# Kernel optimization log

Hardware: AMD Instinct MI355X
Metric: run time of the kernel (lower is better)

The kernel has to match this reference:

```python
import jax, jax.numpy as jnp
import numpy as np

N = 100000   # nodes
E = 800000   # edges
NC = 500     # category nodes
EC = 20000   # category relation edges
D = 64       # out_feats
HOUR_PERIOD = 6  # emb_mix('hour') uses time_period = 6


def l2norm(x):
    # torch F.normalize(p=2, dim=-1) with eps clamp
    return x / jnp.maximum(jnp.linalg.norm(x, axis=-1, keepdims=True), 1e-12)


def proj_transh(x, norm):
    # x - <x, norm> * norm  (per-row)
    return x - jnp.sum(x * norm, axis=-1, keepdims=True) * norm


def edge_softmax(score, dst, n):
    # softmax over incoming edges of each destination node
    m = jax.ops.segment_max(score, dst, num_segments=n)
    e = jnp.exp(score - m[dst])
    s = jax.ops.segment_sum(e, dst, num_segments=n)
    return e / s[dst]


def setup_inputs() -> dict:
    key = jax.random.key(0)
    ks = jax.random.split(key, 12)
    nfeat = jax.random.normal(ks[0], (N, D), dtype=jnp.float32)
    cat_embedding = jax.random.normal(ks[1], (NC, D), dtype=jnp.float32)
    src = jax.random.randint(ks[2], (E,), 0, N, dtype=jnp.int32)
    dst = jax.random.randint(ks[3], (E,), 0, N, dtype=jnp.int32)
    feats_type = jax.random.randint(ks[4], (E,), 0, 7, dtype=jnp.int32)
    hour_id = jax.random.randint(ks[5], (E,), 0, HOUR_PERIOD, dtype=jnp.int32)
    cat_src = jax.random.randint(ks[6], (EC,), 0, NC, dtype=jnp.int32)
    cat_dst = jax.random.randint(ks[7], (EC,), 0, NC, dtype=jnp.int32)
    # learned parameters (embeddings are L2-normalized at init, as in torch code)
    rel_emb = l2norm(jax.random.normal(ks[8], (7, D), dtype=jnp.float32))
    norm_emb = l2norm(jax.random.normal(ks[9], (7, D), dtype=jnp.float32))
    hour_emb = l2norm(jax.random.normal(ks[10], (25, D), dtype=jnp.float32))
    time_rel_w = jax.random.normal(ks[11], (D, D), dtype=jnp.float32) * (1.0 / np.sqrt(D))
    time_rel_b = jnp.zeros((D,), dtype=jnp.float32)
    return {
        "nfeat": nfeat, "cat_embedding": cat_embedding,
        "rel_emb": rel_emb, "norm_emb": norm_emb, "hour_emb": hour_emb,
        "time_rel_w": time_rel_w, "time_rel_b": time_rel_b,
        "src": src, "dst": dst, "feats_type": feats_type, "hour_id": hour_id,
        "cat_src": cat_src, "cat_dst": cat_dst,
    }


def reference(nfeat, cat_embedding, rel_emb, norm_emb, hour_emb,
              time_rel_w, time_rel_b,
              src, dst, feats_type, hour_id, cat_src, cat_dst):
    # ---- category relation graph (cat_emb_type='relation', cat_score_type='transe')
    h_c = cat_embedding[cat_src]                        # [EC, D]
    t_c = cat_embedding[cat_dst]                        # [EC, D]
    rel_c = rel_emb[6]                                  # [D]
    diff_c = h_c + rel_c - t_c
    score_c = jnp.exp(-jnp.sum(diff_c * diff_c, axis=1))  # [EC]
    a_c = edge_softmax(score_c, cat_dst, NC)
    cat_hid = jax.ops.segment_sum(h_c * a_c[:, None], cat_dst, num_segments=NC)

    # ---- main graph edge features
    rel = rel_emb[feats_type]                           # [E, D]
    norm = norm_emb[feats_type]                         # [E, D]
    time_norm = norm_emb[5]                             # [D] (type-5 for all edges)
    # time relation: mixed hour embedding -> linear -> L2 normalize
    last_h = (hour_id - 1 + HOUR_PERIOD) % HOUR_PERIOD
    next_h = (hour_id + 1) % HOUR_PERIOD
    mix = (hour_emb[last_h] + hour_emb[hour_id] + hour_emb[next_h]) / 3.0  # [E, D]
    time_rel = l2norm(mix @ time_rel_w.T + time_rel_b)  # [E, D]

    h = nfeat[src]                                      # [E, D]
    t = nfeat[dst]                                      # [E, D]
    # TransH score on relation hyperplane
    d1 = proj_transh(h, norm) + rel - proj_transh(t, norm)
    score = jnp.exp(-jnp.sum(d1 * d1, axis=1))
    # TransH score on time hyperplane
    d2 = proj_transh(h, time_norm[None, :]) + time_rel - proj_transh(t, time_norm[None, :])
    score_t = jnp.exp(-jnp.sum(d2 * d2, axis=1))
    fin_score = score * score_t                         # [E]

    a = edge_softmax(fin_score, dst, N)                 # [E]
    rst = jax.ops.segment_sum(h * a[:, None], dst, num_segments=N)  # [N, D]
    return rst, cat_hid
```

## Files before the change

kernel.cpp:

```cpp
#include <hip/hip_runtime.h>

#define D 64
#define HOUR_PERIOD 6
#define CAPM 40
#define CAPC 96
#define CSTR 8

__device__ __forceinline__ float bf2f(unsigned short u) {
    union { unsigned int i; float f; } v; v.i = ((unsigned int)u) << 16; return v.f;
}
__device__ __forceinline__ unsigned short f2bf(float f) {
    union { float fl; unsigned int i; } v; v.fl = f;
    unsigned int x = v.i;
    return (unsigned short)((x + 0x7fffu + ((x >> 16) & 1u)) >> 16);
}
__device__ __forceinline__ float4 ld4(const void* base, int idx4, int fp32) {
    if (fp32) return reinterpret_cast<const float4*>(base)[idx4];
    ushort4 u = reinterpret_cast<const ushort4*>(base)[idx4];
    return make_float4(bf2f(u.x), bf2f(u.y), bf2f(u.z), bf2f(u.w));
}
__device__ __forceinline__ float ld1(const void* base, int i, int fp32) {
    return fp32 ? reinterpret_cast<const float*>(base)[i]
                : bf2f(reinterpret_cast<const unsigned short*>(base)[i]);
}
__device__ __forceinline__ void ld8(const void* base, int row, int l, int f,
                                    float& h0, float& h1, float& h2, float& h3,
                                    float& h4, float& h5, float& h6, float& h7) {
    if (f) {
        const float4* p = reinterpret_cast<const float4*>(base) + row * 16 + l * 2;
        float4 u = p[0], v = p[1];
        h0 = u.x; h1 = u.y; h2 = u.z; h3 = u.w;
        h4 = v.x; h5 = v.y; h6 = v.z; h7 = v.w;
    } else {
        uint4 u = reinterpret_cast<const uint4*>(base)[row * 8 + l];
        h0 = bf2f((unsigned short)(u.x & 0xFFFFu)); h1 = bf2f((unsigned short)(u.x >> 16));
        h2 = bf2f((unsigned short)(u.y & 0xFFFFu)); h3 = bf2f((unsigned short)(u.y >> 16));
        h4 = bf2f((unsigned short)(u.z & 0xFFFFu)); h5 = bf2f((unsigned short)(u.z >> 16));
        h6 = bf2f((unsigned short)(u.w & 0xFFFFu)); h7 = bf2f((unsigned short)(u.w >> 16));
    }
}
__device__ __forceinline__ int detect_f(const void* rel_emb) {
    int lane = threadIdx.x & 63;
    float da = bf2f(reinterpret_cast<const unsigned short*>(rel_emb)[lane]);
    float db = bf2f(reinterpret_cast<const unsigned short*>(rel_emb)[lane + 64]);
    int bad = (!(fabsf(da) <= 100.f)) || (!(fabsf(db) <= 100.f));
    unsigned long long m = __ballot(bad);
    return (m != 0ull) ? 1 : 0;
}
__device__ __forceinline__ float wsum64(float v) {
    #pragma unroll
    for (int off = 32; off; off >>= 1) v += __shfl_xor(v, off, 64);
    return v;
}
__device__ __forceinline__ float rsum8(float v) {
    v += __shfl_xor(v, 1, 64);
    v += __shfl_xor(v, 2, 64);
    v += __shfl_xor(v, 4, 64);
    return v;
}

__global__ void k_pp(const int* __restrict__ src, const int* __restrict__ dst,
                     const int* __restrict__ ft, const int* __restrict__ hh,
                     const int* __restrict__ csrc, const int* __restrict__ cdst,
                     int* __restrict__ cnt, unsigned* __restrict__ recsM,
                     unsigned* __restrict__ recsC,
                     const void* __restrict__ nfeat, const void* __restrict__ cemb,
                     const void* __restrict__ rel_emb, const void* __restrict__ norm_emb,
                     const void* __restrict__ hour_emb, const void* __restrict__ trw,
                     const void* __restrict__ trb,
                     unsigned* __restrict__ pmain, float2* __restrict__ pcat,
                     float* __restrict__ consts,
                     int E, int EC, int N, int NC, int GP) {
    __shared__ float vt[20 * D];
    __shared__ float mix6[HOUR_PERIOD * D];
    __shared__ float trwT[D * 65];
    int t = threadIdx.x;
    if (blockIdx.x < GP) {
        int tid = blockIdx.x * 256 + t;
        int mainT = (E + 3) >> 2;
        if (tid < mainT) {
            int e4 = tid * 4;
            if (e4 + 3 < E) {
                int4 s4 = reinterpret_cast<const int4*>(src)[tid];
                int4 d4 = reinterpret_cast<const int4*>(dst)[tid];
                int4 f4 = reinterpret_cast<const int4*>(ft)[tid];
                int4 h4 = reinterpret_cast<const int4*>(hh)[tid];
                int r0 = atomicAdd(&cnt[d4.x * CSTR], 1);
                int r1 = atomicAdd(&cnt[d4.y * CSTR], 1);
                int r2 = atomicAdd(&cnt[d4.z * CSTR], 1);
                int r3 = atomicAdd(&cnt[d4.w * CSTR], 1);
                if (r0 < CAPM) recsM[d4.x * CAPM + r0] = (unsigned)s4.x | ((unsigned)f4.x << 17) | ((unsigned)h4.x << 20);
                if (r1 < CAPM) recsM[d4.y * CAPM + r1] = (unsigned)s4.y | ((unsigned)f4.y << 17) | ((unsigned)h4.y << 20);
                if (r2 < CAPM) recsM[d4.z * CAPM + r2] = (unsigned)s4.z | ((unsigned)f4.z << 17) | ((unsigned)h4.z << 20);
                if (r3 < CAPM) recsM[d4.w * CAPM + r3] = (unsigned)s4.w | ((unsigned)f4.w << 17) | ((unsigned)h4.w << 20);
            } else {
                for (int k = e4; k < E; ++k) {
                    int dv = dst[k];
                    int r = atomicAdd(&cnt[dv * CSTR], 1);
                    if (r < CAPM)
                        recsM[dv * CAPM + r] =
                            (unsigned)src[k] | ((unsigned)ft[k] << 17) | ((unsigned)hh[k] << 20);
                }
            }
        } else {
            int j = tid - mainT, e4 = j * 4;
            if (e4 + 3 < EC) {
                int4 s4 = reinterpret_cast<const int4*>(csrc)[j];
                int4 d4 = reinterpret_cast<const int4*>(cdst)[j];
                int r0 = atomicAdd(&cnt[(N + d4.x) * CSTR], 1);
                int r1 = atomicAdd(&cnt[(N + d4.y) * CSTR], 1);
                int r2 = atomicAdd(&cnt[(N + d4.z) * CSTR], 1);
                int r3 = atomicAdd(&cnt[(N + d4.w) * CSTR], 1);
                if (r0 < CAPC) recsC[d4.x * CAPC + r0] = (unsigned)s4.x;
                if (r1 < CAPC) recsC[d4.y * CAPC + r1] = (unsigned)s4.y;
                if (r2 < CAPC) recsC[d4.z * CAPC + r2] = (unsigned)s4.z;
                if (r3 < CAPC) recsC[d4.w * CAPC + r3] = (unsigned)s4.w;
            } else {
                for (int k = e4; k < EC; ++k) {
                    int dv = cdst[k];
                    int r = atomicAdd(&cnt[(N + dv) * CSTR], 1);
                    if (r < CAPC) recsC[dv * CAPC + r] = (unsigned)csrc[k];
                }
            }
        }
        return;
    }
    int pb = blockIdx.x - GP;
    int f = detect_f(rel_emb);
    int lane = t & 63, w = t >> 6;
    for (int i = t; i < 7 * D; i += 256) vt[i] = ld1(rel_emb, i, f);
    for (int i = t; i < 7 * D; i += 256) vt[7 * D + i] = ld1(norm_emb, i, f);
    for (int i = t; i < HOUR_PERIOD * D; i += 256) {
        int hv = i >> 6, k = i & 63;
        int last = (hv + HOUR_PERIOD - 1) % HOUR_PERIOD, next = (hv + 1) % HOUR_PERIOD;
        mix6[i] = (ld1(hour_emb, last * D + k, f) + ld1(hour_emb, hv * D + k, f) +
                   ld1(hour_emb, next * D + k, f)) * (1.f / 3.f);
    }
    for (int i = t; i < D * D; i += 256)
        trwT[(i & 63) * 65 + (i >> 6)] = ld1(trw, i, f);
    __syncthreads();
    for (int hv = w; hv < HOUR_PERIOD; hv += 4) {
        float y = ld1(trb, lane, f);
        #pragma unroll 4
        for (int kk = 0; kk < D; ++kk) y += mix6[hv * D + kk] * trwT[kk * 65 + lane];
        float ss = wsum64(y * y);
        vt[(14 + hv) * D + lane] = y / fmaxf(sqrtf(ss), 1e-12f);
    }
    __syncthreads();
    int tid = pb * 256 + t;
    if (tid < N) {
        float R0 = 0.f, R1 = 0.f, R2a = 0.f, R3 = 0.f, R4 = 0.f, R5 = 0.f, R6 = 0.f;
        float Nm0 = 0.f, Nm1 = 0.f, Nm2 = 0.f, Nm3 = 0.f, Nm4 = 0.f, Nm5 = 0.f, Nm6 = 0.f;
        float T0 = 0.f, T1 = 0.f, T2 = 0.f, T3 = 0.f, T4 = 0.f, T5 = 0.f;
        float S2 = 0.f;
        const float4* vp = reinterpret_cast<const float4*>(vt);
        #pragma unroll 2
        for (int k4 = 0; k4 < 16; ++k4) {
            float4 x = ld4(nfeat, tid * 16 + k4, f);
            #define DOTV(acc, v) { float4 qv = vp[(v) * 16 + k4]; \
                acc += x.x * qv.x + x.y * qv.y + x.z * qv.z + x.w * qv.w; }
            DOTV(R0, 0)  DOTV(R1, 1)  DOTV(R2a, 2) DOTV(R3, 3)
            DOTV(R4, 4)  DOTV(R5, 5)  DOTV(R6, 6)
            DOTV(Nm0, 7) DOTV(Nm1, 8) DOTV(Nm2, 9) DOTV(Nm3, 10)
            DOTV(Nm4, 11) DOTV(Nm5, 12) DOTV(Nm6, 13)
            DOTV(T0, 14) DOTV(T1, 15) DOTV(T2, 16) DOTV(T3, 17)
            DOTV(T4, 18) DOTV(T5, 19)
            #undef DOTV
            S2 += x.x * x.x + x.y * x.y + x.z * x.z + x.w * x.w;
        }
        unsigned w0 = (unsigned)f2bf(Nm0) | ((unsigned)f2bf(R0) << 16);
        unsigned w1 = (unsigned)f2bf(Nm1) | ((unsigned)f2bf(R1) << 16);
        unsigned w2 = (unsigned)f2bf(Nm2) | ((unsigned)f2bf(R2a) << 16);
        unsigned w3 = (unsigned)f2bf(Nm3) | ((unsigned)f2bf(R3) << 16);
        unsigned w4 = (unsigned)f2bf(Nm4) | ((unsigned)f2bf(R4) << 16);
        unsigned w5 = (unsigned)f2bf(Nm5) | ((unsigned)f2bf(R5) << 16);
        unsigned w6 = (unsigned)f2bf(Nm6) | ((unsigned)f2bf(R6) << 16);
        unsigned w7 = (unsigned)f2bf(T0) | ((unsigned)f2bf(T1) << 16);
        unsigned w8 = (unsigned)f2bf(T2) | ((unsigned)f2bf(T3) << 16);
        unsigned w9 = (unsigned)f2bf(T4) | ((unsigned)f2bf(T5) << 16);
        union { float ff; unsigned u; } cs, ca;
        cs.ff = S2; ca.ff = Nm5;
        uint4* dp = reinterpret_cast<uint4*>(pmain + (size_t)tid * 16);
        dp[0] = make_uint4(w0, w1, w2, w3);
        dp[1] = make_uint4(w4, w5, w6, w7);
        dp[2] = make_uint4(w8, w9, cs.u, ca.u);
        dp[3] = make_uint4(0, 0, 0, 0);
    } else if (tid - N < NC) {
        int i = tid - N;
        float S = 0.f, Cr = 0.f;
        #pragma unroll 4
        for (int k4 = 0; k4 < 16; ++k4) {
            float4 x = ld4(cemb, i * 16 + k4, f);
            float4 rv = *reinterpret_cast<const float4*>(&vt[6 * D + k4 * 4]);
            S  += x.x * x.x + x.y * x.y + x.z * x.z + x.w * x.w;
            Cr += x.x * rv.x + x.y * rv.y + x.z * rv.z + x.w * rv.w;
        }
        pcat[i] = make_float2(S, Cr);
    }
    if (pb == 0) {
        if (t < 7) {
            float R2 = 0.f, RN = 0.f, N2 = 0.f;
            for (int k = 0; k < D; ++k) {
                float r = vt[t * D + k], n = vt[(7 + t) * D + k];
                R2 += r * r; RN += r * n; N2 += n * n;
            }
            consts[t * 4 + 0] = R2; consts[t * 4 + 1] = RN;
            consts[t * 4 + 2] = N2 - 2.f; consts[t * 4 + 3] = 0.f;
        } else if (t < 13) {
            int hv = t - 7;
            float T2c = 0.f, TQ = 0.f;
            for (int k = 0; k < D; ++k) {
                float a = vt[(14 + hv) * D + k], qv = vt[12 * D + k];
                T2c += a * a; TQ += a * qv;
            }
            consts[28 + hv * 2] = T2c; consts[29 + hv * 2] = TQ;
        } else if (t == 13) {
            float Q2 = 0.f;
            for (int k = 0; k < D; ++k) { float qv = vt[12 * D + k]; Q2 += qv * qv; }
            consts[40] = Q2 - 2.f;
        } else if (t == 14) {
            float R = 0.f;
            for (int k = 0; k < D; ++k) { float r = vt[6 * D + k]; R += r * r; }
            consts[41] = R;
        }
    }
}

__launch_bounds__(256, 4)
__global__ void k_fused(const void* __restrict__ nfeat, const void* __restrict__ cemb,
                        const void* __restrict__ rel_emb,
                        const unsigned char* __restrict__ pmain,
                        const float2* __restrict__ pcat,
                        const float* __restrict__ consts,
                        const int* __restrict__ cnt,
                        const unsigned* __restrict__ recsM,
                        const unsigned* __restrict__ recsC,
                        void* __restrict__ out, int N, int M) {
    int t = threadIdx.x;
    int f = detect_f(rel_emb);
    __shared__ __align__(16) float sc[44];
    if (t < 42) sc[t] = consts[t];
    __syncthreads();
    int lane = t & 63, w = t >> 6;
    int l = lane & 7, q = lane >> 3;
    float Q2m2 = sc[40], R2c = sc[41];
    int dbase = (blockIdx.x * 4 + w) * 4;
    for (int d = dbase; d < dbase + 4 && d < M; ++d) {
        float a0 = 0.f, a1 = 0.f, a2 = 0.f, a3 = 0.f;
        float a4 = 0.f, a5 = 0.f, a6 = 0.f, a7 = 0.f, se = 0.f;
        if (d < N) {
            int nE = cnt[d * CSTR]; nE = nE > CAPM ? CAPM : nE;
            int i0 = d * CAPM;
            float t0, t1, t2, t3, t4, t5, t6, t7;
            ld8(nfeat, d, l, f, t0, t1, t2, t3, t4, t5, t6, t7);
            const unsigned char* pd = pmain + (size_t)d * 64;
            float2 sd2 = *reinterpret_cast<const float2*>(pd + 40);
            unsigned pk = (nE > 0) ? recsM[i0 + q] : 0u;
            for (int b = 0; b < nE; b += 8) {
                unsigned pkn = 0u;
                if (b + 8 < nE) pkn = recsM[i0 + b + 8 + q];
                int valid = (b + q) < nE;
                unsigned pkv = valid ? pk : 0u;
                int s = pkv & 0x1FFFF, fv = (pkv >> 17) & 7, hv = (pkv >> 20) & 7;
                const unsigned char* ps = pmain + (size_t)s * 64;
                float h0, h1, h2, h3, h4, h5, h6, h7;
                ld8(nfeat, s, l, f, h0, h1, h2, h3, h4, h5, h6, h7);
                unsigned aws = *reinterpret_cast<const unsigned*>(ps + 4 * fv);
                unsigned short dhs = *reinterpret_cast<const unsigned short*>(ps + 28 + 2 * hv);
                float2 sa = *reinterpret_cast<const float2*>(ps + 40);
                unsigned awd = *reinterpret_cast<const unsigned*>(pd + 4 * fv);
                unsigned short dhd = *reinterpret_cast<const unsigned short*>(pd + 28 + 2 * hv);
                float4 cf  = *reinterpret_cast<float4*>(&sc[fv * 4]);
                float2 cth = *reinterpret_cast<float2*>(&sc[28 + hv * 2]);
                float hdot = rsum8(h0 * t0 + h1 * t1 + h2 * t2 + h3 * t3 +
                                   h4 * t4 + h5 * t5 + h6 * t6 + h7 * t7);
                float As = bf2f((unsigned short)(aws & 0xFFFFu));
                float Cs = bf2f((unsigned short)(aws >> 16));
                float Ad = bf2f((unsigned short)(awd & 0xFFFFu));
                float Cd = bf2f((unsigned short)(awd >> 16));
                float Dhs = bf2f(dhs), Dhd = bf2f(dhd);
                float al = As - Ad;
                float be = sa.y - sd2.y;
                float w2 = sa.x + sd2.x - 2.f * hdot;
                float ssq = 2.f * w2 + cf.x + cth.x + 2.f * (Cs - Cd) + 2.f * (Dhs - Dhd)
                          + al * al * cf.z - 2.f * al * cf.y
                          + be * be * Q2m2 - 2.f * be * cth.y;
                float es = __expf(__expf(-ssq));
                es = valid ? es : 0.f;
                a0 += es * h0; a1 += es * h1; a2 += es * h2; a3 += es * h3;
                a4 += es * h4; a5 += es * h5; a6 += es * h6; a7 += es * h7;
                se += es;
                pk = pkn;
            }
        } else {
            int dc = d - N;
            int nE = cnt[d * CSTR]; nE = nE > CAPC ? CAPC : nE;
            int i0 = dc * CAPC;
            float t0, t1, t2, t3, t4, t5, t6, t7;
            ld8(cemb, dc, l, f, t0, t1, t2, t3, t4, t5, t6, t7);
            float2 td = pcat[dc];
            unsigned pk = (nE > 0) ? recsC[i0 + q] : 0u;
            for (int b = 0; b < nE; b += 8) {
                unsigned pkn = 0u;
                if (b + 8 < nE) pkn = recsC[i0 + b + 8 + q];
                int valid = (b + q) < nE;
                unsigned s = valid ? pk : 0u;
                float h0, h1, h2, h3, h4, h5, h6, h7;
                ld8(cemb, (int)s, l, f, h0, h1, h2, h3, h4, h5, h6, h7);
                float2 csh = pcat[s];
                float hdot = rsum8(h0 * t0 + h1 * t1 + h2 * t2 + h3 * t3 +
                                   h4 * t4 + h5 * t5 + h6 * t6 + h7 * t7);
                float ssq = csh.x + td.x + R2c + 2.f * csh.y - 2.f * td.y - 2.f * hdot;
                float es = __expf(__expf(-ssq));
                es = valid ? es : 0.f;
                a0 += es * h0; a1 += es * h1; a2 += es * h2; a3 += es * h3;
                a4 += es * h4; a5 += es * h5; a6 += es * h6; a7 += es * h7;
                se += es;
                pk = pkn;
            }
        }
        #define RED(x) x += __shfl_xor(x, 8, 64); x += __shfl_xor(x, 16, 64); x += __shfl_xor(x, 32, 64);
        RED(a0) RED(a1) RED(a2) RED(a3) RED(a4) RED(a5) RED(a6) RED(a7) RED(se)
        #undef RED
        float inv = (se > 0.f) ? 1.f / se : 0.f;
        if (q == 0) {
            if (f) {
                float4* op = reinterpret_cast<float4*>(out) + d * 16 + l * 2;
                op[0] = make_float4(a0 * inv, a1 * inv, a2 * inv, a3 * inv);
                op[1] = make_float4(a4 * inv, a5 * inv, a6 * inv, a7 * inv);
            } else {
                unsigned w0 = (unsigned)f2bf(a0 * inv) | ((unsigned)f2bf(a1 * inv) << 16);
                unsigned w1 = (unsigned)f2bf(a2 * inv) | ((unsigned)f2bf(a3 * inv) << 16);
                unsigned w2 = (unsigned)f2bf(a4 * inv) | ((unsigned)f2bf(a5 * inv) << 16);
                unsigned w3 = (unsigned)f2bf(a6 * inv) | ((unsigned)f2bf(a7 * inv) << 16);
                reinterpret_cast<uint4*>(out)[d * 8 + l] = make_uint4(w0, w1, w2, w3);
            }
        }
    }
}

extern "C" void kernel_launch(void* const* d_in, const int* in_sizes, int n_in,
                              void* d_out, int out_size, void* d_ws, size_t ws_size,
                              hipStream_t stream) {
    const void* nfeat    = d_in[0];
    const void* cemb     = d_in[1];
    const void* rel_emb  = d_in[2];
    const void* norm_emb = d_in[3];
    const void* hour_emb = d_in[4];
    const void* trw      = d_in[5];
    const void* trb      = d_in[6];
    const int* src    = (const int*)d_in[7];
    const int* dst    = (const int*)d_in[8];
    const int* ftype  = (const int*)d_in[9];
    const int* hourid = (const int*)d_in[10];
    const int* csrc   = (const int*)d_in[11];
    const int* cdst   = (const int*)d_in[12];

    const int N  = in_sizes[0] / D;
    const int NC = in_sizes[1] / D;
    const int E  = in_sizes[7];
    const int EC = in_sizes[11];
    const int M  = N + NC;

    unsigned char* base = (unsigned char*)d_ws;
    size_t o = 0;
    int* cnt = (int*)(base + o);          o += ((size_t)M * CSTR * 4 + 255) & ~(size_t)255;
    float* consts = (float*)(base + o);   o += 256;
    unsigned* pmain = (unsigned*)(base + o); o += (size_t)N * 64;
    float2* pcat = (float2*)(base + o);   o += ((size_t)NC * 8 + 255) & ~(size_t)255;
    unsigned* recsM = (unsigned*)(base + o); o += (size_t)N * CAPM * 4;
    unsigned* recsC = (unsigned*)(base + o); o += (size_t)NC * CAPC * 4;

    (void)hipMemsetAsync(cnt, 0, (size_t)M * CSTR * 4, stream);

    int histT = (E + 3) / 4 + (EC + 3) / 4;
    int GP    = (histT + 255) / 256;
    int GPREP = (M + 255) / 256;
    k_pp<<<GP + GPREP, 256, 0, stream>>>(src, dst, ftype, hourid, csrc, cdst,
                                         cnt, recsM, recsC,
                                         nfeat, cemb, rel_emb, norm_emb,
                                         hour_emb, trw, trb,
                                         pmain, pcat, consts,
                                         E, EC, N, NC, GP);
    k_fused<<<(M + 15) / 16, 256, 0, stream>>>(nfeat, cemb, rel_emb,
                                               (const unsigned char*)pmain, pcat,
                                               consts, cnt,
                                               recsM, recsC, d_out, N, M);
}
```

Baseline: 239.1 us.

## Reorder prep/histogram blocks, use one edge per thread, drop shared trw transpose

Puts the per-node precompute blocks first in the grid and the edge bucketing blocks after them. Bucketing now handles one edge per thread with scalar loads instead of four edges per thread with int4 loads, which spreads the atomics across more threads. The shared-memory transpose of time_rel_w is removed and the weights are read directly from global memory in the small hour-projection loop, cutting shared memory per block. The trade-off is four times as many bucketing threads, non-vectorized index loads, and strided global reads of trw.

```diff
diff --git a/kernel.cpp b/kernel.cpp
--- a/kernel.cpp
+++ b/kernel.cpp
@@ -70,62 +70,27 @@
                      const void* __restrict__ trb,
                      unsigned* __restrict__ pmain, float2* __restrict__ pcat,
                      float* __restrict__ consts,
-                     int E, int EC, int N, int NC, int GP) {
+                     int E, int EC, int N, int NC, int GPREP) {
     __shared__ float vt[20 * D];
     __shared__ float mix6[HOUR_PERIOD * D];
-    __shared__ float trwT[D * 65];
     int t = threadIdx.x;
-    if (blockIdx.x < GP) {
-        int tid = blockIdx.x * 256 + t;
-        int mainT = (E + 3) >> 2;
-        if (tid < mainT) {
-            int e4 = tid * 4;
-            if (e4 + 3 < E) {
-                int4 s4 = reinterpret_cast<const int4*>(src)[tid];
-                int4 d4 = reinterpret_cast<const int4*>(dst)[tid];
-                int4 f4 = reinterpret_cast<const int4*>(ft)[tid];
-                int4 h4 = reinterpret_cast<const int4*>(hh)[tid];
-                int r0 = atomicAdd(&cnt[d4.x * CSTR], 1);
-                int r1 = atomicAdd(&cnt[d4.y * CSTR], 1);
-                int r2 = atomicAdd(&cnt[d4.z * CSTR], 1);
-                int r3 = atomicAdd(&cnt[d4.w * CSTR], 1);
-                if (r0 < CAPM) recsM[d4.x * CAPM + r0] = (unsigned)s4.x | ((unsigned)f4.x << 17) | ((unsigned)h4.x << 20);
-                if (r1 < CAPM) recsM[d4.y * CAPM + r1] = (unsigned)s4.y | ((unsigned)f4.y << 17) | ((unsigned)h4.y << 20);
-                if (r2 < CAPM) recsM[d4.z * CAPM + r2] = (unsigned)s4.z | ((unsigned)f4.z << 17) | ((unsigned)h4.z << 20);
-                if (r3 < CAPM) recsM[d4.w * CAPM + r3] = (unsigned)s4.w | ((unsigned)f4.w << 17) | ((unsigned)h4.w << 20);
-            } else {
-                for (int k = e4; k < E; ++k) {
-                    int dv = dst[k];
-                    int r = atomicAdd(&cnt[dv * CSTR], 1);
-                    if (r < CAPM)
-                        recsM[dv * CAPM + r] =
-                            (unsigned)src[k] | ((unsigned)ft[k] << 17) | ((unsigned)hh[k] << 20);
-                }
-            }
-        } else {
-            int j = tid - mainT, e4 = j * 4;
-            if (e4 + 3 < EC) {
-                int4 s4 = reinterpret_cast<const int4*>(csrc)[j];
-                int4 d4 = reinterpret_cast<const int4*>(cdst)[j];
-                int r0 = atomicAdd(&cnt[(N + d4.x) * CSTR], 1);
-                int r1 = atomicAdd(&cnt[(N + d4.y) * CSTR], 1);
-                int r2 = atomicAdd(&cnt[(N + d4.z) * CSTR], 1);
-                int r3 = atomicAdd(&cnt[(N + d4.w) * CSTR], 1);
-                if (r0 < CAPC) recsC[d4.x * CAPC + r0] = (unsigned)s4.x;
-                if (r1 < CAPC) recsC[d4.y * CAPC + r1] = (unsigned)s4.y;
-                if (r2 < CAPC) recsC[d4.z * CAPC + r2] = (unsigned)s4.z;
-                if (r3 < CAPC) recsC[d4.w * CAPC + r3] = (unsigned)s4.w;
-            } else {
-                for (int k = e4; k < EC; ++k) {
-                    int dv = cdst[k];
-                    int r = atomicAdd(&cnt[(N + dv) * CSTR], 1);
-                    if (r < CAPC) recsC[dv * CAPC + r] = (unsigned)csrc[k];
-                }
-            }
+    if (blockIdx.x >= GPREP) {
+        int tid = (blockIdx.x - GPREP) * 256 + t;
+        if (tid < E) {
+            int sv = src[tid], dv = dst[tid], fv = ft[tid], hv = hh[tid];
+            int r = atomicAdd(&cnt[dv * CSTR], 1);
+            if (r < CAPM)
+                recsM[dv * CAPM + r] =
+                    (unsigned)sv | ((unsigned)fv << 17) | ((unsigned)hv << 20);
+        } else if (tid - E < EC) {
+            int k = tid - E;
+            int sv = csrc[k], dv = cdst[k];
+            int r = atomicAdd(&cnt[(N + dv) * CSTR], 1);
+            if (r < CAPC) recsC[dv * CAPC + r] = (unsigned)sv;
         }
         return;
     }
-    int pb = blockIdx.x - GP;
+    int pb = blockIdx.x;
     int f = detect_f(rel_emb);
     int lane = t & 63, w = t >> 6;
     for (int i = t; i < 7 * D; i += 256) vt[i] = ld1(rel_emb, i, f);
@@ -136,13 +101,12 @@
         mix6[i] = (ld1(hour_emb, last * D + k, f) + ld1(hour_emb, hv * D + k, f) +
                    ld1(hour_emb, next * D + k, f)) * (1.f / 3.f);
     }
-    for (int i = t; i < D * D; i += 256)
-        trwT[(i & 63) * 65 + (i >> 6)] = ld1(trw, i, f);
     __syncthreads();
     for (int hv = w; hv < HOUR_PERIOD; hv += 4) {
         float y = ld1(trb, lane, f);
         #pragma unroll 4
-        for (int kk = 0; kk < D; ++kk) y += mix6[hv * D + kk] * trwT[kk * 65 + lane];
+        for (int kk = 0; kk < D; ++kk)
+            y += mix6[hv * D + kk] * ld1(trw, lane * D + kk, f);
         float ss = wsum64(y * y);
         vt[(14 + hv) * D + lane] = y / fmaxf(sqrtf(ss), 1e-12f);
     }
@@ -373,15 +337,14 @@
 
     (void)hipMemsetAsync(cnt, 0, (size_t)M * CSTR * 4, stream);
 
-    int histT = (E + 3) / 4 + (EC + 3) / 4;
-    int GP    = (histT + 255) / 256;
+    int GP    = (E + EC + 255) / 256;
     int GPREP = (M + 255) / 256;
-    k_pp<<<GP + GPREP, 256, 0, stream>>>(src, dst, ftype, hourid, csrc, cdst,
+    k_pp<<<GPREP + GP, 256, 0, stream>>>(src, dst, ftype, hourid, csrc, cdst,
                                          cnt, recsM, recsC,
                                          nfeat, cemb, rel_emb, norm_emb,
                                          hour_emb, trw, trb,
                                          pmain, pcat, consts,
-                                         E, EC, N, NC, GP);
+                                         E, EC, N, NC, GPREP);
     k_fused<<<(M + 15) / 16, 256, 0, stream>>>(nfeat, cemb, rel_emb,
                                                (const unsigned char*)pmain, pcat,
                                                consts, cnt,
```

After: 222.7 us. -6.9%, faster.
